# Optimization experiments

Measured on AMD Instinct MI355X. Metric: run time of the kernel, lower is better.

Reference implementation:

```python
import jax, jax.numpy as jnp
import numpy as np
import math

B, SQ, SK, D, H = 2, 2048, 2048, 1024, 16
DH = D // H
EPS = 1e-5

def _ln(x, g, b):
    m = jnp.mean(x, axis=-1, keepdims=True)
    v = jnp.mean(jnp.square(x - m), axis=-1, keepdims=True)
    return (x - m) / jnp.sqrt(v + EPS) * g + b

def setup_inputs() -> dict:
    key = jax.random.key(0)
    ks = jax.random.split(key, 8)
    xav = math.sqrt(6.0 / (D + D))  # xavier_uniform for square [D,D] weights
    inp = {
        'Q': jax.random.normal(ks[0], (B, SQ, D), dtype=jnp.float32),
        'K': jax.random.normal(ks[1], (B, SK, D), dtype=jnp.float32),
        'pad_mask': jax.random.randint(ks[2], (B, SK), 0, 2, dtype=jnp.int32),
        'Wq': jax.random.uniform(ks[3], (D, D), jnp.float32, -xav, xav),
        'Wk': jax.random.uniform(ks[4], (D, D), jnp.float32, -xav, xav),
        'Wv': jax.random.uniform(ks[5], (D, D), jnp.float32, -xav, xav),
        'Wo': jax.random.uniform(ks[6], (D, D), jnp.float32, -xav, xav),
        'bq': jnp.zeros((D,), jnp.float32),
        'bk': jnp.zeros((D,), jnp.float32),
        'bv': jnp.zeros((D,), jnp.float32),
        'bo': jnp.zeros((D,), jnp.float32),
        'ln_q_g': jnp.ones((D,), jnp.float32),  'ln_q_b': jnp.zeros((D,), jnp.float32),
        'ln_kv_g': jnp.ones((D,), jnp.float32), 'ln_kv_b': jnp.zeros((D,), jnp.float32),
        'ln_f_g': jnp.ones((D,), jnp.float32),  'ln_f_b': jnp.zeros((D,), jnp.float32),
    }
    return inp

def reference(Q, K, pad_mask, Wq, Wk, Wv, Wo, bq, bk, bv, bo,
              ln_q_g, ln_q_b, ln_kv_g, ln_kv_b, ln_f_g, ln_f_b):
    Q_ = _ln(Q, ln_q_g, ln_q_b)
    K_ = _ln(K, ln_kv_g, ln_kv_b)
    # projections (PyTorch Linear: x @ W.T + b)
    Q1 = (Q_ @ Wq.T + bq).reshape(B, SQ, H, DH)
    K1 = (K_ @ Wk.T + bk).reshape(B, SK, H, DH)
    V1 = (K_ @ Wv.T + bv).reshape(B, SK, H, DH)
    # note: scaling uses sqrt(dim_V), NOT sqrt(head_dim), per source
    score = jnp.einsum('bqhd,bkhd->bhqk', Q1, K1) / math.sqrt(D)
    m = pad_mask[:, None, None, :]  # [B,1,1,SK]
    score = jnp.where(m == 0, jnp.float32(-1e12), score)
    A = jax.nn.softmax(score, axis=-1)
    A = A * m.astype(A.dtype)  # second mask application after softmax
    O1 = jnp.einsum('bhqk,bkhd->bqhd', A, V1).reshape(B, SQ, D)
    O2 = jax.nn.relu(Q_ @ Wo.T + bo)
    return _ln(Q + O1 + O2, ln_f_g, ln_f_b)
```

## Files before the change

### kernel.cpp

```cpp
#include <hip/hip_runtime.h>
#include <stdint.h>

#define NB 2
#define NSQ 2048
#define NSK 2048
#define ND 1024
#define NH 16
#define NDH 64

typedef unsigned short u16;
typedef unsigned int u32;
typedef __bf16 bf16x8_t __attribute__((ext_vector_type(8)));
typedef float f32x4_t __attribute__((ext_vector_type(4)));
typedef u32 u32x4_t __attribute__((ext_vector_type(4)));
typedef short s16x4 __attribute__((ext_vector_type(4)));
typedef u32 u32x2_t __attribute__((ext_vector_type(2)));

#define AS1 __attribute__((address_space(1)))
#define AS3 __attribute__((address_space(3)))

__device__ __forceinline__ float bf2f(u16 u) {
    union { float f; u32 i; } v; v.i = ((u32)u) << 16; return v.f;
}
__device__ __forceinline__ u16 f2bf(float x) {
    union { float f; u32 i; } v; v.f = x;
    u32 r = v.i + 0x7fffu + ((v.i >> 16) & 1u);
    return (u16)(r >> 16);
}
__device__ __forceinline__ u32 fbits(float x) {
    union { float f; u32 i; } v; v.f = x; return v.i;
}
__device__ __forceinline__ float fexp2(float x) {
#if __has_builtin(__builtin_amdgcn_exp2f)
    return __builtin_amdgcn_exp2f(x);
#else
    return exp2f(x);
#endif
}
__device__ __forceinline__ f32x4_t mfma16(s16x4 a, s16x4 b, f32x4_t c) {
#if __has_builtin(__builtin_amdgcn_mfma_f32_16x16x16bf16_1k)
    return __builtin_amdgcn_mfma_f32_16x16x16bf16_1k(a, b, c, 0, 0, 0);
#else
    asm("v_mfma_f32_16x16x16_bf16 %0, %1, %2, %0" : "+v"(c) : "v"(a), "v"(b));
    return c;
#endif
}
__device__ __forceinline__ int detect_f32(const u16* __restrict__ Q) {
    uint2 x = ((const uint2*)Q)[threadIdx.x & 63];
    u16 a0 = x.x & 0xffff, a1 = x.x >> 16, a2 = x.y & 0xffff, a3 = x.y >> 16;
    bool big = (((a0 >> 7) & 0xff) >= 0x8D) || (((a1 >> 7) & 0xff) >= 0x8D) ||
               (((a2 >> 7) & 0xff) >= 0x8D) || (((a3 >> 7) & 0xff) >= 0x8D);
    return __any(big);
}

#define PREP_LN   (2 * NB * NSQ)
#define PREP_CVT  4106
__global__ __launch_bounds__(256) void prep_kernel(
    const void* __restrict__ Q, const void* __restrict__ K,
    const int* __restrict__ pad_mask,
    const void* __restrict__ Wq, const void* __restrict__ Wk,
    const void* __restrict__ Wv, const void* __restrict__ Wo,
    const void* __restrict__ vbq, const void* __restrict__ vbk,
    const void* __restrict__ vbv, const void* __restrict__ vbo,
    const void* __restrict__ g0, const void* __restrict__ b0,
    const void* __restrict__ g1, const void* __restrict__ b1,
    const void* __restrict__ g2, const void* __restrict__ b2,
    u16* __restrict__ Wc, u16* __restrict__ Vc,
    int* __restrict__ idx, int* __restrict__ cnt,
    u16* __restrict__ Qn, u16* __restrict__ Kn)
{
    int bx = blockIdx.x;
    int t  = threadIdx.x;

    if (bx < PREP_LN) {
        int flag = detect_f32((const u16*)Q);
        int row = bx;
        const void* x; const void *gv, *bv; u16* y;
        size_t roff;
        if (row < NB * NSQ) {
            x = Q; roff = (size_t)row * ND;
            gv = g0; bv = b0;
            y = Qn + roff;
        } else {
            int r2 = row - NB * NSQ;
            x = K; roff = (size_t)r2 * ND;
            gv = g1; bv = b1;
            y = Kn + roff;
        }
        float v0, v1, v2, v3, gg0, gg1, gg2, gg3, bb0, bb1, bb2, bb3;
        if (flag) {
            float4 xv = ((const float4*)x)[roff / 4 + t];
            v0 = xv.x; v1 = xv.y; v2 = xv.z; v3 = xv.w;
            float4 G = ((const float4*)gv)[t];
            float4 Bv = ((const float4*)bv)[t];
            gg0 = G.x; gg1 = G.y; gg2 = G.z; gg3 = G.w;
            bb0 = Bv.x; bb1 = Bv.y; bb2 = Bv.z; bb3 = Bv.w;
        } else {
            uint2 ux = ((const uint2*)x)[roff / 4 + t];
            v0 = bf2f(ux.x & 0xffff); v1 = bf2f(ux.x >> 16);
            v2 = bf2f(ux.y & 0xffff); v3 = bf2f(ux.y >> 16);
            uint2 G = ((const uint2*)gv)[t];
            uint2 Bv = ((const uint2*)bv)[t];
            gg0 = bf2f(G.x & 0xffff); gg1 = bf2f(G.x >> 16);
            gg2 = bf2f(G.y & 0xffff); gg3 = bf2f(G.y >> 16);
            bb0 = bf2f(Bv.x & 0xffff); bb1 = bf2f(Bv.x >> 16);
            bb2 = bf2f(Bv.y & 0xffff); bb3 = bf2f(Bv.y >> 16);
        }
        float s1 = v0 + v1 + v2 + v3;
        float s2 = v0*v0 + v1*v1 + v2*v2 + v3*v3;
#pragma unroll
        for (int off = 32; off >= 1; off >>= 1) {
            s1 += __shfl_xor(s1, off);
            s2 += __shfl_xor(s2, off);
        }
        __shared__ float r1[4], r2[4];
        int wave = t >> 6;
        if ((t & 63) == 0) { r1[wave] = s1; r2[wave] = s2; }
        __syncthreads();
        float t1 = r1[0] + r1[1] + r1[2] + r1[3];
        float t2 = r2[0] + r2[1] + r2[2] + r2[3];
        float mean = t1 * (1.0f / ND);
        float var  = t2 * (1.0f / ND) - mean * mean;
        float rstd = rsqrtf(var + 1e-5f);
        float y0 = (v0 - mean) * rstd * gg0 + bb0;
        float y1 = (v1 - mean) * rstd * gg1 + bb1;
        float y2 = (v2 - mean) * rstd * gg2 + bb2;
        float y3 = (v3 - mean) * rstd * gg3 + bb3;
        uint2 o;
        o.x = (u32)f2bf(y0) | ((u32)f2bf(y1) << 16);
        o.y = (u32)f2bf(y2) | ((u32)f2bf(y3) << 16);
        ((uint2*)y)[t] = o;
    } else if (bx < PREP_LN + PREP_CVT) {
        int flag = detect_f32((const u16*)Q);
        int blk = bx - PREP_LN;
        const void* src;
        u16* dst;
        size_t srcoff;
        if (blk < 4096) {
            int w = blk >> 10;
            src = (w == 0) ? Wq : (w == 1) ? Wk : (w == 2) ? Wv : Wo;
            srcoff = (size_t)(blk & 1023) * 1024;
            dst = Wc + (size_t)w * 1024 * 1024 + srcoff;
        } else {
            int v = blk - 4096;
            src = (v == 0) ? vbq : (v == 1) ? vbk : (v == 2) ? vbv : (v == 3) ? vbo :
                  (v == 4) ? g0  : (v == 5) ? b0  : (v == 6) ? g1  : (v == 7) ? b1 :
                  (v == 8) ? g2  : b2;
            srcoff = 0;
            dst = Vc + (size_t)v * 1024;
        }
        u32 lo, hi;
        if (flag) {
            float4 x = ((const float4*)src)[srcoff / 4 + t];
            lo = (u32)f2bf(x.x) | ((u32)f2bf(x.y) << 16);
            hi = (u32)f2bf(x.z) | ((u32)f2bf(x.w) << 16);
        } else {
            uint2 x = ((const uint2*)src)[srcoff / 4 + t];
            lo = x.x; hi = x.y;
        }
        uint2 o; o.x = lo; o.y = hi;
        ((uint2*)dst)[t] = o;
    } else {
        int b = bx - (PREP_LN + PREP_CVT);
        const int* m = pad_mask + b * NSK;
        int loc[8]; int s = 0;
#pragma unroll
        for (int i = 0; i < 8; ++i) { loc[i] = (m[t * 8 + i] != 0); s += loc[i]; }
        __shared__ int ps[256];
        ps[t] = s;
        __syncthreads();
        for (int off = 1; off < 256; off <<= 1) {
            int v = (t >= off) ? ps[t - off] : 0;
            __syncthreads();
            ps[t] += v;
            __syncthreads();
        }
        int run = ps[t] - s;
#pragma unroll
        for (int i = 0; i < 8; ++i)
            if (loc[i]) idx[b * NSK + run++] = t * 8 + i;
        if (t == 255) cnt[b] = ps[255];
    }
}

__global__ __launch_bounds__(512, 2) void gemm4_kernel(
    const u16* __restrict__ Qn, const u16* __restrict__ Kn,
    const u16* __restrict__ Wc, const u16* __restrict__ Vc,
    u16* __restrict__ Q1, u16* __restrict__ K1, u16* __restrict__ V1,
    u16* __restrict__ R)
{
    int lin = blockIdx.x + 16 * blockIdx.y + 64 * blockIdx.z;
    int u   = (lin & 7) * 32 + (lin >> 3);
    int bx  = u & 15;
    int by  = (u >> 4) & 3;
    int z   = u >> 6;

    const u16* X    = (z == 0 || z == 3) ? Qn : Kn;
    const u16* W    = Wc + (size_t)z * 1024 * 1024;
    const u16* bias = Vc + (size_t)z * 1024;

    __shared__ u16 sm[4][2][256 * 32];

    int tid  = threadIdx.x;
    int wave = tid >> 6, lane = tid & 63;
    int wm = wave >> 2, wn = wave & 3;
    int quad = lane >> 4, l4 = lane & 15;
    int m0 = bx * 256;
    int n0 = by * 256;

    int srow   = wave * 16 + (lane >> 2);
    int schunk = (lane & 3) ^ ((srow >> 1) & 3);
    const u16* gA = X + (size_t)(m0 + srow) * ND + schunk * 8;
    const u16* gB = W + (size_t)(n0 + srow) * ND + schunk * 8;

#define STAGE_A(t_) do { int s_ = (t_) & 3; \
    __builtin_amdgcn_global_load_lds((const AS1 u32*)(gA + (t_) * 32), \
        (AS3 u32*)(&sm[s_][0][wave * 512]), 16, 0, 0); \
    __builtin_amdgcn_global_load_lds((const AS1 u32*)(gA + (t_) * 32 + (size_t)128 * ND), \
        (AS3 u32*)(&sm[s_][0][4096 + wave * 512]), 16, 0, 0); \
} while (0)
#define STAGE_B(t_) do { int s_ = (t_) & 3; \
    __builtin_amdgcn_global_load_lds((const AS1 u32*)(gB + (t_) * 32), \
        (AS3 u32*)(&sm[s_][1][wave * 512]), 16, 0, 0); \
    __builtin_amdgcn_global_load_lds((const AS1 u32*)(gB + (t_) * 32 + (size_t)128 * ND), \
        (AS3 u32*)(&sm[s_][1][4096 + wave * 512]), 16, 0, 0); \
} while (0)

    int fch   = (quad ^ ((l4 >> 1) & 3)) * 8;
    int aoffb = (wm * 128 + l4) * 32 + fch;
    int boffb = (wn * 64  + l4) * 32 + fch;

    f32x4_t acc[8][4];
#pragma unroll
    for (int i = 0; i < 8; ++i)
#pragma unroll
        for (int j = 0; j < 4; ++j)
            acc[i][j] = (f32x4_t){0.f, 0.f, 0.f, 0.f};

    STAGE_A(0); STAGE_B(0);
    STAGE_A(1); STAGE_B(1);
    STAGE_A(2); STAGE_B(2);
    asm volatile("s_waitcnt vmcnt(8)" ::: "memory");
    __builtin_amdgcn_s_barrier();
    __builtin_amdgcn_sched_barrier(0);

    for (int t = 0; t < 32; ++t) {
        const u16* a = &sm[t & 3][0][0];
        const u16* b = &sm[t & 3][1][0];
        bf16x8_t bf[4], af[4], ah[4];

#pragma unroll
        for (int nf = 0; nf < 4; ++nf)
            bf[nf] = *(const bf16x8_t*)(b + boffb + nf * 512);
#pragma unroll
        for (int mf = 0; mf < 4; ++mf)
            af[mf] = *(const bf16x8_t*)(a + aoffb + mf * 512);
#pragma unroll
        for (int mf = 0; mf < 4; ++mf)
            ah[mf] = *(const bf16x8_t*)(a + aoffb + (mf + 4) * 512);

        if (t < 29) { STAGE_A(t + 3); STAGE_B(t + 3); }

        __builtin_amdgcn_s_setprio(1);
#pragma unroll
        for (int mf = 0; mf < 4; ++mf)
#pragma unroll
            for (int nf = 0; nf < 4; ++nf)
                acc[mf][nf] = __builtin_amdgcn_mfma_f32_16x16x32_bf16(
                    af[mf], bf[nf], acc[mf][nf], 0, 0, 0);
#pragma unroll
        for (int mf = 0; mf < 4; ++mf)
#pragma unroll
            for (int nf = 0; nf < 4; ++nf)
                acc[mf + 4][nf] = __builtin_amdgcn_mfma_f32_16x16x32_bf16(
                    ah[mf], bf[nf], acc[mf + 4][nf], 0, 0, 0);
        __builtin_amdgcn_s_setprio(0);

        if (t < 29)       asm volatile("s_waitcnt vmcnt(8)" ::: "memory");
        else if (t == 29) asm volatile("s_waitcnt vmcnt(4)" ::: "memory");
        else if (t == 30) asm volatile("s_waitcnt vmcnt(0)" ::: "memory");
        __builtin_amdgcn_s_barrier();
        __builtin_amdgcn_sched_barrier(0);
    }
#undef STAGE_A
#undef STAGE_B

    u16* outp = (z == 0) ? Q1 : (z == 1) ? K1 : (z == 2) ? V1 : R;
    float bv_[4];
#pragma unroll
    for (int nf = 0; nf < 4; ++nf)
        bv_[nf] = bf2f(bias[n0 + wn * 64 + nf * 16 + l4]);
#pragma unroll
    for (int mf = 0; mf < 8; ++mf) {
#pragma unroll
        for (int r = 0; r < 4; ++r) {
            int m = m0 + wm * 128 + mf * 16 + quad * 4 + r;
#pragma unroll
            for (int nf = 0; nf < 4; ++nf) {
                int n = n0 + wn * 64 + nf * 16 + l4;
                float val = acc[mf][nf][r] + bv_[nf];
                if (z == 0) val *= 0.045105964f;
                if (z == 3) val = fmaxf(val, 0.f);
                outp[(size_t)m * ND + n] = f2bf(val);
            }
        }
    }
}

__global__ __launch_bounds__(256) void gather_kernel(
    const u16* __restrict__ K1, const u16* __restrict__ V1,
    const int* __restrict__ idx, const int* __restrict__ cnt,
    u16* __restrict__ Kc, u16* __restrict__ Vct)
{
    int b = blockIdx.y;
    int c = cnt[b];
    int cPad = (c + 63) & ~63;
    int tid = threadIdx.x;

    if (blockIdx.x < 128) {
        int jb = blockIdx.x * 16;
        if (jb >= cPad) return;
        int row = tid >> 4;
        int seg = tid & 15;
        int j = jb + row;
        if (j >= cPad) return;
        bool z = (j >= c);
        const u16* src = z ? (const u16*)0
            : K1 + ((size_t)b * NSK + idx[(size_t)b * NSK + j]) * ND;
        u16* dst = Kc + ((size_t)b * NSK + j) * ND;
#pragma unroll
        for (int i = 0; i < 8; ++i) {
            int off = (seg * 8 + i) * 8;
            uint4 v = z ? (uint4){0, 0, 0, 0} : *(const uint4*)(src + off);
            *(uint4*)(dst + off) = v;
        }
    } else {
        int lin = blockIdx.x - 128;
        int kb = lin & 31;
        int h  = lin >> 5;
        if (kb * 64 >= cPad) return;
        __shared__ u16 sT[64 * 72];
        {
            int row = tid >> 3, seg = tid & 7;
            int j1 = kb * 64 + row, j2 = j1 + 32;
            uint4 v1 = {0, 0, 0, 0}, v2 = {0, 0, 0, 0};
            if (j1 < c) v1 = *(const uint4*)(V1 +
                ((size_t)b * NSK + idx[(size_t)b * NSK + j1]) * ND + h * NDH + seg * 8);
            if (j2 < c) v2 = *(const uint4*)(V1 +
                ((size_t)b * NSK + idx[(size_t)b * NSK + j2]) * ND + h * NDH + seg * 8);
            *(uint4*)(sT + row * 72 + seg * 8) = v1;
            *(uint4*)(sT + (row + 32) * 72 + seg * 8) = v2;
        }
        __syncthreads();
        int d = tid >> 2, sg = tid & 3;
        u16 buf[16];
#pragma unroll
        for (int i = 0; i < 8; ++i) buf[i]     = sT[(sg * 8 + i) * 72 + d];
#pragma unroll
        for (int i = 0; i < 8; ++i) buf[8 + i] = sT[((sg + 4) * 8 + i) * 72 + d];
        u16* go = Vct + ((size_t)(b * NH + h) * NDH + d) * NSK + kb * 64;
        *(uint4*)(go + sg * 8)       = *(uint4*)buf;
        *(uint4*)(go + (sg + 4) * 8) = *(uint4*)(buf + 8);
    }
}

__global__ __launch_bounds__(256, 4) void attn_kernel(
    const u16* __restrict__ Q1, const u16* __restrict__ Kc,
    const u16* __restrict__ Vct, const int* __restrict__ cnt,
    u16* __restrict__ R)
{
    int q0 = blockIdx.x * 64;
    int h  = blockIdx.y;
    int b  = blockIdx.z;

    __shared__ u16 sK[2][64 * 64];
    __shared__ u16 sV[2][64 * 64];

    int tid  = threadIdx.x;
    int wave = tid >> 6, lane = tid & 63;
    int quad = lane >> 4, l4 = lane & 15;
    int lk = lane >> 3, ls = lane & 7;
    int gseg = ls ^ lk;

    int c  = cnt[b];
    int nt = (c + 63) >> 6;

    bf16x8_t qf[2];
    {
        const u16* qp = Q1 + (size_t)(b * NSQ + q0 + wave * 16 + l4) * ND + h * NDH;
        qf[0] = *(const bf16x8_t*)(qp + quad * 8);
        qf[1] = *(const bf16x8_t*)(qp + 32 + quad * 8);
    }

    const u16* kbase = Kc + (size_t)b * NSK * ND + h * NDH;
    const u16* vbase = Vct + (size_t)(b * NH + h) * NDH * NSK;

    const u16* gk0 = kbase + (size_t)(wave * 16 + lk) * ND + gseg * 8;
    const u16* gk1 = gk0 + (size_t)8 * ND;
    const u16* gv0 = vbase + (size_t)(wave * 16 + lk) * NSK + gseg * 8;
    const u16* gv1 = gv0 + (size_t)8 * NSK;

    int fragOff[2];
#pragma unroll
    for (int kk = 0; kk < 2; ++kk)
        fragOff[kk] = l4 * 64 + (((kk * 4 + quad) ^ (l4 & 7)) * 8);

    int v4off[4];
#pragma unroll
    for (int tm = 0; tm < 4; ++tm)
        v4off[tm] = l4 * 64 + (((2 * tm + (quad >> 1)) ^ (l4 & 7)) * 8)
                  + (quad & 1) * 4;

    float l_run = 0.f;
    f32x4_t acc_o[4];
#pragma unroll
    for (int T = 0; T < 4; ++T) acc_o[T] = (f32x4_t){0.f, 0.f, 0.f, 0.f};

    if (nt > 0) {
        __builtin_amdgcn_global_load_lds((const AS1 u32*)gk0,
            (AS3 u32*)(&sK[0][(wave * 16) * 64]), 16, 0, 0);
        __builtin_amdgcn_global_load_lds((const AS1 u32*)gk1,
            (AS3 u32*)(&sK[0][(wave * 16 + 8) * 64]), 16, 0, 0);
        __builtin_amdgcn_global_load_lds((const AS1 u32*)gv0,
            (AS3 u32*)(&sV[0][(wave * 16) * 64]), 16, 0, 0);
        __builtin_amdgcn_global_load_lds((const AS1 u32*)gv1,
            (AS3 u32*)(&sV[0][(wave * 16 + 8) * 64]), 16, 0, 0);
        gk0 += (size_t)64 * ND; gk1 += (size_t)64 * ND;
        gv0 += 64; gv1 += 64;

        for (int kb = 0; kb < nt; ++kb) {
            __syncthreads();

            if (kb + 1 < nt) {
                int bi = (kb + 1) & 1;
                __builtin_amdgcn_global_load_lds((const AS1 u32*)gk0,
                    (AS3 u32*)(&sK[bi][(wave * 16) * 64]), 16, 0, 0);
                __builtin_amdgcn_global_load_lds((const AS1 u32*)gk1,
                    (AS3 u32*)(&sK[bi][(wave * 16 + 8) * 64]), 16, 0, 0);
                __builtin_amdgcn_global_load_lds((const AS1 u32*)gv0,
                    (AS3 u32*)(&sV[bi][(wave * 16) * 64]), 16, 0, 0);
                __builtin_amdgcn_global_load_lds((const AS1 u32*)gv1,
                    (AS3 u32*)(&sV[bi][(wave * 16 + 8) * 64]), 16, 0, 0);
                gk0 += (size_t)64 * ND; gk1 += (size_t)64 * ND;
                gv0 += 64; gv1 += 64;
            }

            const u16* kt = sK[kb & 1];
            const u16* vt = sV[kb & 1];

            f32x4_t accs[4];
            if (kb == nt - 1) {
#pragma unroll
                for (int tm = 0; tm < 4; ++tm) {
                    int key = kb * 64 + tm * 16 + quad * 4;
#pragma unroll
                    for (int r = 0; r < 4; ++r)
                        accs[tm][r] = (key + r < c) ? 0.f : -1e9f;
                }
            } else {
#pragma unroll
                for (int tm = 0; tm < 4; ++tm)
                    accs[tm] = (f32x4_t){0.f, 0.f, 0.f, 0.f};
            }
#pragma unroll
            for (int kk = 0; kk < 2; ++kk)
#pragma unroll
                for (int tm = 0; tm < 4; ++tm) {
                    bf16x8_t kf = *(const bf16x8_t*)(kt + tm * 1024 + fragOff[kk]);
                    accs[tm] = __builtin_amdgcn_mfma_f32_16x16x32_bf16(
                        kf, qf[kk], accs[tm], 0, 0, 0);
                }

            float lsum = 0.f;
#pragma unroll
            for (int tm = 0; tm < 4; ++tm) {
                float p0 = fexp2(accs[tm][0]);
                float p1 = fexp2(accs[tm][1]);
                float p2 = fexp2(accs[tm][2]);
                float p3 = fexp2(accs[tm][3]);
                lsum += (p0 + p1) + (p2 + p3);
                u32 lo = __builtin_amdgcn_perm(fbits(p1), fbits(p0), 0x07060302);
                u32 hi = __builtin_amdgcn_perm(fbits(p3), fbits(p2), 0x07060302);
                s16x4 pf = __builtin_bit_cast(s16x4, (u32x2_t){lo, hi});
#pragma unroll
                for (int T = 0; T < 4; ++T) {
                    s16x4 vf = *(const s16x4*)(vt + T * 1024 + v4off[tm]);
                    acc_o[T] = mfma16(vf, pf, acc_o[T]);
                }
            }
            lsum += __shfl_xor(lsum, 16);
            lsum += __shfl_xor(lsum, 32);
            l_run += lsum;
        }
    }

    float inv = l_run > 0.f ? 1.f / l_run : 0.f;
    u16* rp = R + (size_t)(b * NSQ + q0 + wave * 16 + l4) * ND + h * NDH;
#pragma unroll
    for (int T = 0; T < 4; ++T) {
        u16* p = rp + T * 16 + quad * 4;
        uint2 o2 = *(const uint2*)p;
        float e0 = acc_o[T][0] * inv + bf2f(o2.x & 0xffff);
        float e1 = acc_o[T][1] * inv + bf2f(o2.x >> 16);
        float e2 = acc_o[T][2] * inv + bf2f(o2.y & 0xffff);
        float e3 = acc_o[T][3] * inv + bf2f(o2.y >> 16);
        uint2 on;
        on.x = (u32)f2bf(e0) | ((u32)f2bf(e1) << 16);
        on.y = (u32)f2bf(e2) | ((u32)f2bf(e3) << 16);
        *(uint2*)p = on;
    }
}

__global__ __launch_bounds__(256) void ln_out_kernel(
    const void* __restrict__ Q, const u16* __restrict__ R,
    const u16* __restrict__ Vc, void* __restrict__ out)
{
    int row = blockIdx.x;
    size_t roff = (size_t)row * ND;
    int t = threadIdx.x;
    int f = detect_f32((const u16*)Q);
    float v0, v1, v2, v3;
    uint2 ur = ((const uint2*)(R + roff))[t];
    if (f) {
        float4 xq = ((const float4*)Q)[roff / 4 + t];
        v0 = xq.x; v1 = xq.y; v2 = xq.z; v3 = xq.w;
    } else {
        uint2 uq = ((const uint2*)Q)[roff / 4 + t];
        v0 = bf2f(uq.x & 0xffff); v1 = bf2f(uq.x >> 16);
        v2 = bf2f(uq.y & 0xffff); v3 = bf2f(uq.y >> 16);
    }
    v0 += bf2f(ur.x & 0xffff); v1 += bf2f(ur.x >> 16);
    v2 += bf2f(ur.y & 0xffff); v3 += bf2f(ur.y >> 16);
    float s1 = v0 + v1 + v2 + v3;
    float s2 = v0*v0 + v1*v1 + v2*v2 + v3*v3;
#pragma unroll
    for (int off = 32; off >= 1; off >>= 1) {
        s1 += __shfl_xor(s1, off);
        s2 += __shfl_xor(s2, off);
    }
    __shared__ float r1[4], r2[4];
    int wave = t >> 6;
    if ((t & 63) == 0) { r1[wave] = s1; r2[wave] = s2; }
    __syncthreads();
    float t1 = r1[0] + r1[1] + r1[2] + r1[3];
    float t2 = r2[0] + r2[1] + r2[2] + r2[3];
    float mean = t1 * (1.0f / ND);
    float var  = t2 * (1.0f / ND) - mean * mean;
    float rstd = rsqrtf(var + 1e-5f);
    const u16* g  = Vc + 8 * 1024;
    const u16* bb = Vc + 9 * 1024;
    uint2 ug = ((const uint2*)g)[t];
    uint2 ub = ((const uint2*)bb)[t];
    float y0 = (v0 - mean) * rstd * bf2f(ug.x & 0xffff) + bf2f(ub.x & 0xffff);
    float y1 = (v1 - mean) * rstd * bf2f(ug.x >> 16)    + bf2f(ub.x >> 16);
    float y2 = (v2 - mean) * rstd * bf2f(ug.y & 0xffff) + bf2f(ub.y & 0xffff);
    float y3 = (v3 - mean) * rstd * bf2f(ug.y >> 16)    + bf2f(ub.y >> 16);
    if (f) {
        float4 o; o.x = y0; o.y = y1; o.z = y2; o.w = y3;
        ((float4*)out)[roff / 4 + t] = o;
    } else {
        uint2 o;
        o.x = (u32)f2bf(y0) | ((u32)f2bf(y1) << 16);
        o.y = (u32)f2bf(y2) | ((u32)f2bf(y3) << 16);
        ((uint2*)out)[roff / 4 + t] = o;
    }
}

extern "C" void kernel_launch(void* const* d_in, const int* in_sizes, int n_in,
                              void* d_out, int out_size, void* d_ws, size_t ws_size,
                              hipStream_t stream) {
    const void* Q        = d_in[0];
    const void* K        = d_in[1];
    const int* pad_mask  = (const int*)d_in[2];

    const size_t NEL = (size_t)NB * NSQ * ND;
    int* flag = (int*)d_ws;
    int* cnt  = flag + 1;
    int* idx  = flag + 4;
    u16* base = (u16*)(idx + 4096);
    u16* Qn  = base;
    u16* Kn  = Qn + NEL;
    u16* Q1  = Kn + NEL;
    u16* K1  = Q1 + NEL;
    u16* V1  = K1 + NEL;
    u16* R   = V1 + NEL;
    u16* Wc  = R + NEL;
    u16* Vc  = Wc + (size_t)4 * 1024 * 1024;
    u16* Kc  = Qn;
    u16* Vct = Kn;

    prep_kernel<<<dim3(PREP_LN + PREP_CVT + NB), dim3(256), 0, stream>>>(
        Q, K, pad_mask,
        d_in[3], d_in[4], d_in[5], d_in[6],
        d_in[7], d_in[8], d_in[9], d_in[10],
        d_in[11], d_in[12], d_in[13], d_in[14], d_in[15], d_in[16],
        Wc, Vc, idx, cnt, Qn, Kn);

    gemm4_kernel<<<dim3(16, 4, 4), dim3(512), 0, stream>>>(
        Qn, Kn, Wc, Vc, Q1, K1, V1, R);

    gather_kernel<<<dim3(128 + 32 * NH, NB), dim3(256), 0, stream>>>(
        K1, V1, idx, cnt, Kc, Vct);

    attn_kernel<<<dim3(NSQ / 64, NH, NB), dim3(256), 0, stream>>>(
        Q1, Kc, Vct, cnt, R);

    ln_out_kernel<<<dim3(NB * NSQ), dim3(256), 0, stream>>>(
        Q, R, Vc, d_out);
}
```

Measured before the change: 213.7 us.

## Use 4 waves with 128x128 warp tiles in projection GEMM

The projection GEMM kernel goes from 8 waves per 256x256 block to 4 waves, each computing a 128x128 sub-tile with an 8x8 grid of MFMA accumulators. Each wave now issues four global-to-LDS loads per operand per stage, the wait counts are adjusted to match, and the LDS swizzle term is recomputed from the lane index. The aim is more MFMA work per LDS fragment read and fewer waves contending, in exchange for much higher register pressure (256 accumulator floats per lane) and lower occupancy.

```diff
diff --git a/kernel.cpp b/kernel.cpp
--- a/kernel.cpp
+++ b/kernel.cpp
@@ -183,7 +183,7 @@
     }
 }
 
-__global__ __launch_bounds__(512, 2) void gemm4_kernel(
+__global__ __launch_bounds__(256, 1) void gemm4_kernel(
     const u16* __restrict__ Qn, const u16* __restrict__ Kn,
     const u16* __restrict__ Wc, const u16* __restrict__ Vc,
     u16* __restrict__ Q1, u16* __restrict__ K1, u16* __restrict__ V1,
@@ -203,81 +203,74 @@
 
     int tid  = threadIdx.x;
     int wave = tid >> 6, lane = tid & 63;
-    int wm = wave >> 2, wn = wave & 3;
+    int wm = wave >> 1, wn = wave & 1;
     int quad = lane >> 4, l4 = lane & 15;
     int m0 = bx * 256;
     int n0 = by * 256;
 
     int srow   = wave * 16 + (lane >> 2);
-    int schunk = (lane & 3) ^ ((srow >> 1) & 3);
+    int schunk = (lane & 3) ^ ((lane >> 3) & 3);
     const u16* gA = X + (size_t)(m0 + srow) * ND + schunk * 8;
     const u16* gB = W + (size_t)(n0 + srow) * ND + schunk * 8;
 
 #define STAGE_A(t_) do { int s_ = (t_) & 3; \
-    __builtin_amdgcn_global_load_lds((const AS1 u32*)(gA + (t_) * 32), \
-        (AS3 u32*)(&sm[s_][0][wave * 512]), 16, 0, 0); \
-    __builtin_amdgcn_global_load_lds((const AS1 u32*)(gA + (t_) * 32 + (size_t)128 * ND), \
-        (AS3 u32*)(&sm[s_][0][4096 + wave * 512]), 16, 0, 0); \
+    _Pragma("unroll") \
+    for (int i_ = 0; i_ < 4; ++i_) \
+        __builtin_amdgcn_global_load_lds( \
+            (const AS1 u32*)(gA + (size_t)(t_) * 32 + (size_t)(i_ * 64) * ND), \
+            (AS3 u32*)(&sm[s_][0][i_ * 2048 + wave * 512]), 16, 0, 0); \
 } while (0)
 #define STAGE_B(t_) do { int s_ = (t_) & 3; \
-    __builtin_amdgcn_global_load_lds((const AS1 u32*)(gB + (t_) * 32), \
-        (AS3 u32*)(&sm[s_][1][wave * 512]), 16, 0, 0); \
-    __builtin_amdgcn_global_load_lds((const AS1 u32*)(gB + (t_) * 32 + (size_t)128 * ND), \
-        (AS3 u32*)(&sm[s_][1][4096 + wave * 512]), 16, 0, 0); \
+    _Pragma("unroll") \
+    for (int i_ = 0; i_ < 4; ++i_) \
+        __builtin_amdgcn_global_load_lds( \
+            (const AS1 u32*)(gB + (size_t)(t_) * 32 + (size_t)(i_ * 64) * ND), \
+            (AS3 u32*)(&sm[s_][1][i_ * 2048 + wave * 512]), 16, 0, 0); \
 } while (0)
 
     int fch   = (quad ^ ((l4 >> 1) & 3)) * 8;
     int aoffb = (wm * 128 + l4) * 32 + fch;
-    int boffb = (wn * 64  + l4) * 32 + fch;
-
-    f32x4_t acc[8][4];
+    int boffb = (wn * 128 + l4) * 32 + fch;
+
+    f32x4_t acc[8][8];
 #pragma unroll
     for (int i = 0; i < 8; ++i)
 #pragma unroll
-        for (int j = 0; j < 4; ++j)
+        for (int j = 0; j < 8; ++j)
             acc[i][j] = (f32x4_t){0.f, 0.f, 0.f, 0.f};
 
     STAGE_A(0); STAGE_B(0);
     STAGE_A(1); STAGE_B(1);
     STAGE_A(2); STAGE_B(2);
-    asm volatile("s_waitcnt vmcnt(8)" ::: "memory");
+    asm volatile("s_waitcnt vmcnt(16)" ::: "memory");
     __builtin_amdgcn_s_barrier();
     __builtin_amdgcn_sched_barrier(0);
 
     for (int t = 0; t < 32; ++t) {
         const u16* a = &sm[t & 3][0][0];
         const u16* b = &sm[t & 3][1][0];
-        bf16x8_t bf[4], af[4], ah[4];
-
-#pragma unroll
-        for (int nf = 0; nf < 4; ++nf)
+        bf16x8_t bf[8], af[8];
+
+#pragma unroll
+        for (int nf = 0; nf < 8; ++nf)
             bf[nf] = *(const bf16x8_t*)(b + boffb + nf * 512);
 #pragma unroll
-        for (int mf = 0; mf < 4; ++mf)
+        for (int mf = 0; mf < 8; ++mf)
             af[mf] = *(const bf16x8_t*)(a + aoffb + mf * 512);
-#pragma unroll
-        for (int mf = 0; mf < 4; ++mf)
-            ah[mf] = *(const bf16x8_t*)(a + aoffb + (mf + 4) * 512);
 
         if (t < 29) { STAGE_A(t + 3); STAGE_B(t + 3); }
 
         __builtin_amdgcn_s_setprio(1);
 #pragma unroll
-        for (int mf = 0; mf < 4; ++mf)
-#pragma unroll
-            for (int nf = 0; nf < 4; ++nf)
+        for (int mf = 0; mf < 8; ++mf)
+#pragma unroll
+            for (int nf = 0; nf < 8; ++nf)
                 acc[mf][nf] = __builtin_amdgcn_mfma_f32_16x16x32_bf16(
                     af[mf], bf[nf], acc[mf][nf], 0, 0, 0);
-#pragma unroll
-        for (int mf = 0; mf < 4; ++mf)
-#pragma unroll
-            for (int nf = 0; nf < 4; ++nf)
-                acc[mf + 4][nf] = __builtin_amdgcn_mfma_f32_16x16x32_bf16(
-                    ah[mf], bf[nf], acc[mf + 4][nf], 0, 0, 0);
         __builtin_amdgcn_s_setprio(0);
 
-        if (t < 29)       asm volatile("s_waitcnt vmcnt(8)" ::: "memory");
-        else if (t == 29) asm volatile("s_waitcnt vmcnt(4)" ::: "memory");
+        if (t < 29)       asm volatile("s_waitcnt vmcnt(16)" ::: "memory");
+        else if (t == 29) asm volatile("s_waitcnt vmcnt(8)" ::: "memory");
         else if (t == 30) asm volatile("s_waitcnt vmcnt(0)" ::: "memory");
         __builtin_amdgcn_s_barrier();
         __builtin_amdgcn_sched_barrier(0);
@@ -286,18 +279,18 @@
 #undef STAGE_B
 
     u16* outp = (z == 0) ? Q1 : (z == 1) ? K1 : (z == 2) ? V1 : R;
-    float bv_[4];
-#pragma unroll
-    for (int nf = 0; nf < 4; ++nf)
-        bv_[nf] = bf2f(bias[n0 + wn * 64 + nf * 16 + l4]);
+    float bv_[8];
+#pragma unroll
+    for (int nf = 0; nf < 8; ++nf)
+        bv_[nf] = bf2f(bias[n0 + wn * 128 + nf * 16 + l4]);
 #pragma unroll
     for (int mf = 0; mf < 8; ++mf) {
 #pragma unroll
         for (int r = 0; r < 4; ++r) {
             int m = m0 + wm * 128 + mf * 16 + quad * 4 + r;
 #pragma unroll
-            for (int nf = 0; nf < 4; ++nf) {
-                int n = n0 + wn * 64 + nf * 16 + l4;
+            for (int nf = 0; nf < 8; ++nf) {
+                int n = n0 + wn * 128 + nf * 16 + l4;
                 float val = acc[mf][nf][r] + bv_[nf];
                 if (z == 0) val *= 0.045105964f;
                 if (z == 3) val = fmaxf(val, 0.f);
@@ -596,7 +589,7 @@
         d_in[11], d_in[12], d_in[13], d_in[14], d_in[15], d_in[16],
         Wc, Vc, idx, cnt, Qn, Kn);
 
-    gemm4_kernel<<<dim3(16, 4, 4), dim3(512), 0, stream>>>(
+    gemm4_kernel<<<dim3(16, 4, 4), dim3(256), 0, stream>>>(
         Qn, Kn, Wc, Vc, Q1, K1, V1, R);
 
     gather_kernel<<<dim3(128 + 32 * NH, NB), dim3(256), 0, stream>>>(
```

Result: slower. 230.9 us (+8.1%).

## Fuse final layernorm into attention kernel via last-head-block atomic counter

Applied to the files above, without the earlier changes.

Removes the separate ln_out kernel. Each attention block bumps a per-(batch, query-tile) counter, and the block that finishes the last of the 16 heads runs the residual-add layernorm for those 64 rows. This saves one launch and lets the final layernorm overlap with other attention blocks still running. In exchange, a few blocks do serial tail work of 16 rows per wave with a single wave per row, and the change adds threadfence and atomic overhead.

```diff
diff --git a/kernel.cpp b/kernel.cpp
--- a/kernel.cpp
+++ b/kernel.cpp
@@ -66,7 +66,7 @@
     const void* __restrict__ g1, const void* __restrict__ b1,
     const void* __restrict__ g2, const void* __restrict__ b2,
     u16* __restrict__ Wc, u16* __restrict__ Vc,
-    int* __restrict__ idx, int* __restrict__ cnt,
+    int* __restrict__ idx, int* __restrict__ cnt, int* __restrict__ qcnt,
     u16* __restrict__ Qn, u16* __restrict__ Kn)
 {
     int bx = blockIdx.x;
@@ -162,6 +162,7 @@
         ((uint2*)dst)[t] = o;
     } else {
         int b = bx - (PREP_LN + PREP_CVT);
+        if (t < 32) qcnt[b * 32 + t] = 0;
         const int* m = pad_mask + b * NSK;
         int loc[8]; int s = 0;
 #pragma unroll
@@ -367,7 +368,9 @@
 __global__ __launch_bounds__(256, 4) void attn_kernel(
     const u16* __restrict__ Q1, const u16* __restrict__ Kc,
     const u16* __restrict__ Vct, const int* __restrict__ cnt,
-    u16* __restrict__ R)
+    u16* __restrict__ R,
+    const void* __restrict__ Qraw, const u16* __restrict__ Vc,
+    int* __restrict__ qcnt, void* __restrict__ out)
 {
     int q0 = blockIdx.x * 64;
     int h  = blockIdx.y;
@@ -509,60 +512,72 @@
         on.y = (u32)f2bf(e2) | ((u32)f2bf(e3) << 16);
         *(uint2*)p = on;
     }
-}
-
-__global__ __launch_bounds__(256) void ln_out_kernel(
-    const void* __restrict__ Q, const u16* __restrict__ R,
-    const u16* __restrict__ Vc, void* __restrict__ out)
-{
-    int row = blockIdx.x;
-    size_t roff = (size_t)row * ND;
-    int t = threadIdx.x;
-    int f = detect_f32((const u16*)Q);
-    float v0, v1, v2, v3;
-    uint2 ur = ((const uint2*)(R + roff))[t];
-    if (f) {
-        float4 xq = ((const float4*)Q)[roff / 4 + t];
-        v0 = xq.x; v1 = xq.y; v2 = xq.z; v3 = xq.w;
-    } else {
-        uint2 uq = ((const uint2*)Q)[roff / 4 + t];
-        v0 = bf2f(uq.x & 0xffff); v1 = bf2f(uq.x >> 16);
-        v2 = bf2f(uq.y & 0xffff); v3 = bf2f(uq.y >> 16);
-    }
-    v0 += bf2f(ur.x & 0xffff); v1 += bf2f(ur.x >> 16);
-    v2 += bf2f(ur.y & 0xffff); v3 += bf2f(ur.y >> 16);
-    float s1 = v0 + v1 + v2 + v3;
-    float s2 = v0*v0 + v1*v1 + v2*v2 + v3*v3;
-#pragma unroll
-    for (int off = 32; off >= 1; off >>= 1) {
-        s1 += __shfl_xor(s1, off);
-        s2 += __shfl_xor(s2, off);
-    }
-    __shared__ float r1[4], r2[4];
-    int wave = t >> 6;
-    if ((t & 63) == 0) { r1[wave] = s1; r2[wave] = s2; }
+
+    __threadfence();
     __syncthreads();
-    float t1 = r1[0] + r1[1] + r1[2] + r1[3];
-    float t2 = r2[0] + r2[1] + r2[2] + r2[3];
-    float mean = t1 * (1.0f / ND);
-    float var  = t2 * (1.0f / ND) - mean * mean;
-    float rstd = rsqrtf(var + 1e-5f);
-    const u16* g  = Vc + 8 * 1024;
-    const u16* bb = Vc + 9 * 1024;
-    uint2 ug = ((const uint2*)g)[t];
-    uint2 ub = ((const uint2*)bb)[t];
-    float y0 = (v0 - mean) * rstd * bf2f(ug.x & 0xffff) + bf2f(ub.x & 0xffff);
-    float y1 = (v1 - mean) * rstd * bf2f(ug.x >> 16)    + bf2f(ub.x >> 16);
-    float y2 = (v2 - mean) * rstd * bf2f(ug.y & 0xffff) + bf2f(ub.y & 0xffff);
-    float y3 = (v3 - mean) * rstd * bf2f(ug.y >> 16)    + bf2f(ub.y >> 16);
-    if (f) {
-        float4 o; o.x = y0; o.y = y1; o.z = y2; o.w = y3;
-        ((float4*)out)[roff / 4 + t] = o;
-    } else {
-        uint2 o;
-        o.x = (u32)f2bf(y0) | ((u32)f2bf(y1) << 16);
-        o.y = (u32)f2bf(y2) | ((u32)f2bf(y3) << 16);
-        ((uint2*)out)[roff / 4 + t] = o;
+    __shared__ int sdone;
+    if (tid == 0)
+        sdone = (atomicAdd(&qcnt[b * 32 + blockIdx.x], 1) == NH - 1) ? 1 : 0;
+    __syncthreads();
+    if (!sdone) return;
+    __threadfence();
+
+    int f = detect_f32((const u16*)Qraw);
+    const u16* gg = Vc + 8 * 1024;
+    const u16* gb = Vc + 9 * 1024;
+#pragma unroll 1
+    for (int rr = 0; rr < 16; ++rr) {
+        int row = q0 + rr * 4 + wave;
+        size_t roff = ((size_t)b * NSQ + row) * ND;
+        float v[16];
+#pragma unroll
+        for (int i = 0; i < 4; ++i) {
+            size_t u2i = roff / 4 + i * 64 + lane;
+            uint2 ur = ((const uint2*)R)[u2i];
+            float r0 = bf2f(ur.x & 0xffff), r1 = bf2f(ur.x >> 16);
+            float r2 = bf2f(ur.y & 0xffff), r3 = bf2f(ur.y >> 16);
+            if (f) {
+                float4 xq = ((const float4*)Qraw)[u2i];
+                v[i*4+0] = xq.x + r0; v[i*4+1] = xq.y + r1;
+                v[i*4+2] = xq.z + r2; v[i*4+3] = xq.w + r3;
+            } else {
+                uint2 uq = ((const uint2*)Qraw)[u2i];
+                v[i*4+0] = bf2f(uq.x & 0xffff) + r0;
+                v[i*4+1] = bf2f(uq.x >> 16)    + r1;
+                v[i*4+2] = bf2f(uq.y & 0xffff) + r2;
+                v[i*4+3] = bf2f(uq.y >> 16)    + r3;
+            }
+        }
+        float s1 = 0.f, s2 = 0.f;
+#pragma unroll
+        for (int i = 0; i < 16; ++i) { s1 += v[i]; s2 += v[i] * v[i]; }
+#pragma unroll
+        for (int off = 32; off >= 1; off >>= 1) {
+            s1 += __shfl_xor(s1, off);
+            s2 += __shfl_xor(s2, off);
+        }
+        float mean = s1 * (1.0f / ND);
+        float var  = s2 * (1.0f / ND) - mean * mean;
+        float rstd = rsqrtf(var + 1e-5f);
+#pragma unroll
+        for (int i = 0; i < 4; ++i) {
+            size_t u2i = roff / 4 + i * 64 + lane;
+            uint2 ug = ((const uint2*)gg)[i * 64 + lane];
+            uint2 ub = ((const uint2*)gb)[i * 64 + lane];
+            float y0 = (v[i*4+0] - mean) * rstd * bf2f(ug.x & 0xffff) + bf2f(ub.x & 0xffff);
+            float y1 = (v[i*4+1] - mean) * rstd * bf2f(ug.x >> 16)    + bf2f(ub.x >> 16);
+            float y2 = (v[i*4+2] - mean) * rstd * bf2f(ug.y & 0xffff) + bf2f(ub.y & 0xffff);
+            float y3 = (v[i*4+3] - mean) * rstd * bf2f(ug.y >> 16)    + bf2f(ub.y >> 16);
+            if (f) {
+                float4 o; o.x = y0; o.y = y1; o.z = y2; o.w = y3;
+                ((float4*)out)[u2i] = o;
+            } else {
+                uint2 o;
+                o.x = (u32)f2bf(y0) | ((u32)f2bf(y1) << 16);
+                o.y = (u32)f2bf(y2) | ((u32)f2bf(y3) << 16);
+                ((uint2*)out)[u2i] = o;
+            }
+        }
     }
 }
 
@@ -577,7 +592,8 @@
     int* flag = (int*)d_ws;
     int* cnt  = flag + 1;
     int* idx  = flag + 4;
-    u16* base = (u16*)(idx + 4096);
+    int* qcnt = flag + 4100;
+    u16* base = (u16*)(flag + 4168);
     u16* Qn  = base;
     u16* Kn  = Qn + NEL;
     u16* Q1  = Kn + NEL;
@@ -594,7 +610,7 @@
         d_in[3], d_in[4], d_in[5], d_in[6],
         d_in[7], d_in[8], d_in[9], d_in[10],
         d_in[11], d_in[12], d_in[13], d_in[14], d_in[15], d_in[16],
-        Wc, Vc, idx, cnt, Qn, Kn);
+        Wc, Vc, idx, cnt, qcnt, Qn, Kn);
 
     gemm4_kernel<<<dim3(16, 4, 4), dim3(512), 0, stream>>>(
         Qn, Kn, Wc, Vc, Q1, K1, V1, R);
@@ -603,8 +619,5 @@
         K1, V1, idx, cnt, Kc, Vct);
 
     attn_kernel<<<dim3(NSQ / 64, NH, NB), dim3(256), 0, stream>>>(
-        Q1, Kc, Vct, cnt, R);
-
-    ln_out_kernel<<<dim3(NB * NSQ), dim3(256), 0, stream>>>(
-        Q, R, Vc, d_out);
-}
+        Q1, Kc, Vct, cnt, R, Q, Vc, qcnt, d_out);
+}
```

Measured after the change: 381.0 us. +78.3%, slower.

## Compact unmasked K rows during LayerNorm and skip padded K/V projection tiles

Applied to the files above, without the earlier changes.

Each K LayerNorm block now computes its destination row from a prefix count of the pad mask and writes only unmasked rows, compacted, into Kn. The tail up to a 64-row boundary is zero-filled. The K/V projection GEMM blocks beyond the padded valid count exit early, and the separate K gather pass and index array are removed, so attention reads K1 directly. This removes roughly half the K/V projection work plus a gather copy. In exchange every K-row block scans up to 2048 mask entries, and the pad zeroing runs concurrently with the LN writes in the same kernel.

```diff
diff --git a/kernel.cpp b/kernel.cpp
--- a/kernel.cpp
+++ b/kernel.cpp
@@ -66,26 +66,38 @@
     const void* __restrict__ g1, const void* __restrict__ b1,
     const void* __restrict__ g2, const void* __restrict__ b2,
     u16* __restrict__ Wc, u16* __restrict__ Vc,
-    int* __restrict__ idx, int* __restrict__ cnt,
+    int* __restrict__ cnt,
     u16* __restrict__ Qn, u16* __restrict__ Kn)
 {
     int bx = blockIdx.x;
     int t  = threadIdx.x;
 
     if (bx < PREP_LN) {
+        __shared__ float r1[4], r2[4];
+        __shared__ int r0[4];
         int flag = detect_f32((const u16*)Q);
-        int row = bx;
-        const void* x; const void *gv, *bv; u16* y;
+        int wave = t >> 6;
+        bool isQ = bx < NB * NSQ;
+        int pc = 0;
+        const void* x; const void *gv, *bv;
         size_t roff;
-        if (row < NB * NSQ) {
-            x = Q; roff = (size_t)row * ND;
+        int bb_ = 0;
+        if (isQ) {
+            x = Q; roff = (size_t)bx * ND;
             gv = g0; bv = b0;
-            y = Qn + roff;
         } else {
-            int r2 = row - NB * NSQ;
-            x = K; roff = (size_t)r2 * ND;
+            int r2_ = bx - NB * NSQ;
+            bb_ = r2_ >> 11;
+            int lr = r2_ & 2047;
+            const int* mb = pad_mask + (size_t)bb_ * NSK;
+            if (mb[lr] == 0) return;
+#pragma unroll
+            for (int i = 0; i < 8; ++i) {
+                int j = t * 8 + i;
+                pc += (j < lr && mb[j] != 0) ? 1 : 0;
+            }
+            x = K; roff = ((size_t)bb_ * NSK + lr) * ND;
             gv = g1; bv = b1;
-            y = Kn + roff;
         }
         float v0, v1, v2, v3, gg0, gg1, gg2, gg3, bb0, bb1, bb2, bb3;
         if (flag) {
@@ -112,16 +124,22 @@
         for (int off = 32; off >= 1; off >>= 1) {
             s1 += __shfl_xor(s1, off);
             s2 += __shfl_xor(s2, off);
-        }
-        __shared__ float r1[4], r2[4];
-        int wave = t >> 6;
-        if ((t & 63) == 0) { r1[wave] = s1; r2[wave] = s2; }
+            pc += __shfl_xor(pc, off);
+        }
+        if ((t & 63) == 0) { r1[wave] = s1; r2[wave] = s2; r0[wave] = pc; }
         __syncthreads();
         float t1 = r1[0] + r1[1] + r1[2] + r1[3];
         float t2 = r2[0] + r2[1] + r2[2] + r2[3];
         float mean = t1 * (1.0f / ND);
         float var  = t2 * (1.0f / ND) - mean * mean;
         float rstd = rsqrtf(var + 1e-5f);
+        u16* y;
+        if (isQ) {
+            y = Qn + (size_t)bx * ND;
+        } else {
+            int dst = r0[0] + r0[1] + r0[2] + r0[3];
+            y = Kn + ((size_t)bb_ * NSK + dst) * ND;
+        }
         float y0 = (v0 - mean) * rstd * gg0 + bb0;
         float y1 = (v1 - mean) * rstd * gg1 + bb1;
         float y2 = (v2 - mean) * rstd * gg2 + bb2;
@@ -162,30 +180,30 @@
         ((uint2*)dst)[t] = o;
     } else {
         int b = bx - (PREP_LN + PREP_CVT);
-        const int* m = pad_mask + b * NSK;
-        int loc[8]; int s = 0;
-#pragma unroll
-        for (int i = 0; i < 8; ++i) { loc[i] = (m[t * 8 + i] != 0); s += loc[i]; }
-        __shared__ int ps[256];
-        ps[t] = s;
+        const int* m = pad_mask + (size_t)b * NSK;
+        int s = 0;
+#pragma unroll
+        for (int i = 0; i < 8; ++i) s += (m[t * 8 + i] != 0) ? 1 : 0;
+#pragma unroll
+        for (int off = 32; off >= 1; off >>= 1) s += __shfl_xor(s, off);
+        __shared__ int rs[4];
+        int wave = t >> 6;
+        if ((t & 63) == 0) rs[wave] = s;
         __syncthreads();
-        for (int off = 1; off < 256; off <<= 1) {
-            int v = (t >= off) ? ps[t - off] : 0;
-            __syncthreads();
-            ps[t] += v;
-            __syncthreads();
-        }
-        int run = ps[t] - s;
-#pragma unroll
-        for (int i = 0; i < 8; ++i)
-            if (loc[i]) idx[b * NSK + run++] = t * 8 + i;
-        if (t == 255) cnt[b] = ps[255];
+        int c = rs[0] + rs[1] + rs[2] + rs[3];
+        if (t == 0) cnt[b] = c;
+        int cPad = (c + 63) & ~63;
+        int nel = (cPad - c) * ND;
+        u16* zp = Kn + ((size_t)b * NSK + c) * ND;
+        for (int e = t * 8; e < nel; e += 256 * 8)
+            *(uint4*)(zp + e) = (uint4){0, 0, 0, 0};
     }
 }
 
 __global__ __launch_bounds__(512, 2) void gemm4_kernel(
     const u16* __restrict__ Qn, const u16* __restrict__ Kn,
     const u16* __restrict__ Wc, const u16* __restrict__ Vc,
+    const int* __restrict__ cnt,
     u16* __restrict__ Q1, u16* __restrict__ K1, u16* __restrict__ V1,
     u16* __restrict__ R)
 {
@@ -194,6 +212,12 @@
     int bx  = u & 15;
     int by  = (u >> 4) & 3;
     int z   = u >> 6;
+
+    if (z == 1 || z == 2) {
+        int batch = bx >> 3;
+        int cPad  = (cnt[batch] + 63) & ~63;
+        if ((bx & 7) * 256 >= cPad) return;
+    }
 
     const u16* X    = (z == 0 || z == 3) ? Qn : Kn;
     const u16* W    = Wc + (size_t)z * 1024 * 1024;
@@ -307,65 +331,40 @@
     }
 }
 
-__global__ __launch_bounds__(256) void gather_kernel(
-    const u16* __restrict__ K1, const u16* __restrict__ V1,
-    const int* __restrict__ idx, const int* __restrict__ cnt,
-    u16* __restrict__ Kc, u16* __restrict__ Vct)
+__global__ __launch_bounds__(256) void gather_vt_kernel(
+    const u16* __restrict__ V1, const int* __restrict__ cnt,
+    u16* __restrict__ Vct)
 {
-    int b = blockIdx.y;
+    int kb = blockIdx.x & 31;
+    int h  = blockIdx.x >> 5;
+    int b  = blockIdx.y;
     int c = cnt[b];
     int cPad = (c + 63) & ~63;
+    if (kb * 64 >= cPad) return;
+    __shared__ u16 sT[64 * 72];
     int tid = threadIdx.x;
-
-    if (blockIdx.x < 128) {
-        int jb = blockIdx.x * 16;
-        if (jb >= cPad) return;
-        int row = tid >> 4;
-        int seg = tid & 15;
-        int j = jb + row;
-        if (j >= cPad) return;
-        bool z = (j >= c);
-        const u16* src = z ? (const u16*)0
-            : K1 + ((size_t)b * NSK + idx[(size_t)b * NSK + j]) * ND;
-        u16* dst = Kc + ((size_t)b * NSK + j) * ND;
-#pragma unroll
-        for (int i = 0; i < 8; ++i) {
-            int off = (seg * 8 + i) * 8;
-            uint4 v = z ? (uint4){0, 0, 0, 0} : *(const uint4*)(src + off);
-            *(uint4*)(dst + off) = v;
-        }
-    } else {
-        int lin = blockIdx.x - 128;
-        int kb = lin & 31;
-        int h  = lin >> 5;
-        if (kb * 64 >= cPad) return;
-        __shared__ u16 sT[64 * 72];
-        {
-            int row = tid >> 3, seg = tid & 7;
-            int j1 = kb * 64 + row, j2 = j1 + 32;
-            uint4 v1 = {0, 0, 0, 0}, v2 = {0, 0, 0, 0};
-            if (j1 < c) v1 = *(const uint4*)(V1 +
-                ((size_t)b * NSK + idx[(size_t)b * NSK + j1]) * ND + h * NDH + seg * 8);
-            if (j2 < c) v2 = *(const uint4*)(V1 +
-                ((size_t)b * NSK + idx[(size_t)b * NSK + j2]) * ND + h * NDH + seg * 8);
-            *(uint4*)(sT + row * 72 + seg * 8) = v1;
-            *(uint4*)(sT + (row + 32) * 72 + seg * 8) = v2;
-        }
-        __syncthreads();
-        int d = tid >> 2, sg = tid & 3;
-        u16 buf[16];
-#pragma unroll
-        for (int i = 0; i < 8; ++i) buf[i]     = sT[(sg * 8 + i) * 72 + d];
-#pragma unroll
-        for (int i = 0; i < 8; ++i) buf[8 + i] = sT[((sg + 4) * 8 + i) * 72 + d];
-        u16* go = Vct + ((size_t)(b * NH + h) * NDH + d) * NSK + kb * 64;
-        *(uint4*)(go + sg * 8)       = *(uint4*)buf;
-        *(uint4*)(go + (sg + 4) * 8) = *(uint4*)(buf + 8);
-    }
+    {
+        int row = tid >> 3, seg = tid & 7;
+        int j1 = kb * 64 + row, j2 = j1 + 32;
+        uint4 v1 = *(const uint4*)(V1 + ((size_t)b * NSK + j1) * ND + h * NDH + seg * 8);
+        uint4 v2 = *(const uint4*)(V1 + ((size_t)b * NSK + j2) * ND + h * NDH + seg * 8);
+        *(uint4*)(sT + row * 72 + seg * 8) = v1;
+        *(uint4*)(sT + (row + 32) * 72 + seg * 8) = v2;
+    }
+    __syncthreads();
+    int d = tid >> 2, sg = tid & 3;
+    u16 buf[16];
+#pragma unroll
+    for (int i = 0; i < 8; ++i) buf[i]     = sT[(sg * 8 + i) * 72 + d];
+#pragma unroll
+    for (int i = 0; i < 8; ++i) buf[8 + i] = sT[((sg + 4) * 8 + i) * 72 + d];
+    u16* go = Vct + ((size_t)(b * NH + h) * NDH + d) * NSK + kb * 64;
+    *(uint4*)(go + sg * 8)       = *(uint4*)buf;
+    *(uint4*)(go + (sg + 4) * 8) = *(uint4*)(buf + 8);
 }
 
 __global__ __launch_bounds__(256, 4) void attn_kernel(
-    const u16* __restrict__ Q1, const u16* __restrict__ Kc,
+    const u16* __restrict__ Q1, const u16* __restrict__ K1c,
     const u16* __restrict__ Vct, const int* __restrict__ cnt,
     u16* __restrict__ R)
 {
@@ -392,7 +391,7 @@
         qf[1] = *(const bf16x8_t*)(qp + 32 + quad * 8);
     }
 
-    const u16* kbase = Kc + (size_t)b * NSK * ND + h * NDH;
+    const u16* kbase = K1c + (size_t)b * NSK * ND + h * NDH;
     const u16* vbase = Vct + (size_t)(b * NH + h) * NDH * NSK;
 
     const u16* gk0 = kbase + (size_t)(wave * 16 + lk) * ND + gseg * 8;
@@ -576,8 +575,7 @@
     const size_t NEL = (size_t)NB * NSQ * ND;
     int* flag = (int*)d_ws;
     int* cnt  = flag + 1;
-    int* idx  = flag + 4;
-    u16* base = (u16*)(idx + 4096);
+    u16* base = (u16*)(flag + 4168);
     u16* Qn  = base;
     u16* Kn  = Qn + NEL;
     u16* Q1  = Kn + NEL;
@@ -586,7 +584,6 @@
     u16* R   = V1 + NEL;
     u16* Wc  = R + NEL;
     u16* Vc  = Wc + (size_t)4 * 1024 * 1024;
-    u16* Kc  = Qn;
     u16* Vct = Kn;
 
     prep_kernel<<<dim3(PREP_LN + PREP_CVT + NB), dim3(256), 0, stream>>>(
@@ -594,16 +591,16 @@
         d_in[3], d_in[4], d_in[5], d_in[6],
         d_in[7], d_in[8], d_in[9], d_in[10],
         d_in[11], d_in[12], d_in[13], d_in[14], d_in[15], d_in[16],
-        Wc, Vc, idx, cnt, Qn, Kn);
+        Wc, Vc, cnt, Qn, Kn);
 
     gemm4_kernel<<<dim3(16, 4, 4), dim3(512), 0, stream>>>(
-        Qn, Kn, Wc, Vc, Q1, K1, V1, R);
-
-    gather_kernel<<<dim3(128 + 32 * NH, NB), dim3(256), 0, stream>>>(
-        K1, V1, idx, cnt, Kc, Vct);
+        Qn, Kn, Wc, Vc, cnt, Q1, K1, V1, R);
+
+    gather_vt_kernel<<<dim3(32 * NH, NB), dim3(256), 0, stream>>>(
+        V1, cnt, Vct);
 
     attn_kernel<<<dim3(NSQ / 64, NH, NB), dim3(256), 0, stream>>>(
-        Q1, Kc, Vct, cnt, R);
+        Q1, K1, Vct, cnt, R);
 
     ln_out_kernel<<<dim3(NB * NSQ), dim3(256), 0, stream>>>(
         Q, R, Vc, d_out);
```

Result: no change. 217.3 us (+1.7%).
